# Optimization experiments

Measured on AMD Instinct MI355X. Metric: run time of the kernel, lower is better.

The kernel has to match this reference:

```python
import jax, jax.numpy as jnp
import numpy as np

B, S, D, H = 2, 2048, 1024, 16
HD = D // H
EPS = 1e-5


def setup_inputs() -> dict:
    key = jax.random.key(0)
    ks = jax.random.split(key, 8)
    std = 1.0 / np.sqrt(D)
    x = jax.random.normal(ks[0], (B, S, D), dtype=jnp.float32)
    # causal mask: True = attend (masked_fill where mask==0)
    attention_mask = jnp.tril(jnp.ones((S, S), dtype=bool))[None, None].repeat(B, axis=0)
    return {
        "x": x,
        "attention_mask": attention_mask,
        "ln_gamma": jnp.ones((D,), jnp.float32),
        "ln_beta": jnp.zeros((D,), jnp.float32),
        "w_qkv": jax.random.uniform(ks[1], (D, 3 * D), jnp.float32, -std, std),
        "b_qkv": jnp.zeros((3 * D,), jnp.float32),
        "w_gate": jax.random.uniform(ks[2], (D, D), jnp.float32, -std, std),
        "b_gate": jnp.zeros((D,), jnp.float32),
        "w_out": jax.random.uniform(ks[3], (D, D), jnp.float32, -std, std),
        "b_out": jnp.zeros((D,), jnp.float32),
        "rel_pos_bias": jnp.zeros((1, H, 1, 1), jnp.float32),
    }


def reference(x, attention_mask, ln_gamma, ln_beta, w_qkv, b_qkv,
              w_gate, b_gate, w_out, b_out, rel_pos_bias):
    # LayerNorm over model dim
    mu = jnp.mean(x, axis=-1, keepdims=True)
    var = jnp.mean(jnp.square(x - mu), axis=-1, keepdims=True)
    xn = (x - mu) * jax.lax.rsqrt(var + EPS) * ln_gamma + ln_beta

    qkv = xn @ w_qkv + b_qkv                      # [B,S,3D]
    qkv = qkv.reshape(B, S, 3, H, HD)
    q = qkv[:, :, 0].transpose(0, 2, 1, 3)        # [B,H,S,HD]
    k = qkv[:, :, 1].transpose(0, 2, 1, 3)
    v = qkv[:, :, 2].transpose(0, 2, 1, 3)

    u = jax.nn.silu(xn @ w_gate + b_gate)         # [B,S,D] SiLU gate

    scale = HD ** -0.5
    scores = jnp.einsum('bhqd,bhkd->bhqk', q * scale, k) + rel_pos_bias
    # masked_fill(mask==0, -inf) then sigmoid == zero out masked entries
    attn = jnp.where(attention_mask, jax.nn.sigmoid(scores), 0.0)
    ctx = jnp.einsum('bhqk,bhkd->bhqd', attn, v)  # [B,H,S,HD]
    ctx = ctx.transpose(0, 2, 1, 3).reshape(B, S, D)

    out = (ctx * u) @ w_out + b_out               # gated output proj
    return x + out                                # dropout=eval identity
```

## Files before the change

kernel.cpp:

```cpp
#include <hip/hip_runtime.h>
#include <hip/hip_bf16.h>
#include <cmath>

#define BB 2
#define SS 2048
#define DD 1024
#define HH 16
#define EPS 1e-5f
#define LOG2E 1.44269504088896f
#define QSCALE (0.125f * LOG2E)

typedef __attribute__((ext_vector_type(8))) short short8;
typedef __attribute__((ext_vector_type(4))) float f32x4;

__device__ inline unsigned short f2bf(float f) {
  union { float f; unsigned int u; } v; v.f = f;
  unsigned int u = v.u;
  unsigned int r = (u + 0x7FFFu + ((u >> 16) & 1u)) >> 16;
  return (unsigned short)r;
}
__device__ inline float bf2f(unsigned short h) {
  union { unsigned int u; float f; } v; v.u = ((unsigned int)h) << 16;
  return v.f;
}
__device__ inline unsigned short f2bf_fast(float f) {
  union { float f; unsigned int u; } v; v.f = f;
  return (unsigned short)((v.u + 0x8000u) >> 16);
}

__global__ __launch_bounds__(256) void ln_kernel(
    const float* __restrict__ x, const float* __restrict__ gamma,
    const float* __restrict__ beta, unsigned short* __restrict__ xn) {
  int row = blockIdx.x;
  int t = threadIdx.x;
  const float* xr = x + (size_t)row * DD;
  float4 v = *(const float4*)(xr + t * 4);
  float s = v.x + v.y + v.z + v.w;
  float sq = v.x * v.x + v.y * v.y + v.z * v.z + v.w * v.w;
  for (int off = 32; off > 0; off >>= 1) {
    s += __shfl_down(s, off, 64);
    sq += __shfl_down(sq, off, 64);
  }
  __shared__ float ls[4], lq[4];
  int wave = t >> 6, lane = t & 63;
  if (lane == 0) { ls[wave] = s; lq[wave] = sq; }
  __syncthreads();
  float tot = ls[0] + ls[1] + ls[2] + ls[3];
  float totq = lq[0] + lq[1] + lq[2] + lq[3];
  float mu = tot * (1.0f / DD);
  float var = totq * (1.0f / DD) - mu * mu;
  float rstd = rsqrtf(var + EPS);
  float4 g = *(const float4*)(gamma + t * 4);
  float4 bt = *(const float4*)(beta + t * 4);
  ushort4 o;
  o.x = f2bf((v.x - mu) * rstd * g.x + bt.x);
  o.y = f2bf((v.y - mu) * rstd * g.y + bt.y);
  o.z = f2bf((v.z - mu) * rstd * g.z + bt.z);
  o.w = f2bf((v.w - mu) * rstd * g.w + bt.w);
  *(ushort4*)(xn + (size_t)row * DD + t * 4) = o;
}

__global__ __launch_bounds__(256) void wtrans_all(
    const float* __restrict__ wq, const float* __restrict__ wg,
    const float* __restrict__ wo, unsigned short* __restrict__ wcatT,
    unsigned short* __restrict__ woutT) {
  __shared__ unsigned short tile[32][33];
  int bx = blockIdx.x;
  const float* W;
  unsigned short* Wt;
  int N, colbase;
  if (bx < 96)       { W = wq; Wt = wcatT; N = 3072; colbase = bx * 32; }
  else if (bx < 128) { W = wg; Wt = wcatT + (size_t)3072 * 1024; N = 1024; colbase = (bx - 96) * 32; }
  else               { W = wo; Wt = woutT; N = 1024; colbase = (bx - 128) * 32; }
  int by = blockIdx.y * 32;
  int tx = threadIdx.x & 31, ty = threadIdx.x >> 5;
#pragma unroll
  for (int i = 0; i < 32; i += 8)
    tile[ty + i][tx] = f2bf(W[(size_t)(by + ty + i) * N + colbase + tx]);
  __syncthreads();
#pragma unroll
  for (int i = 0; i < 32; i += 8)
    Wt[(size_t)(colbase + ty + i) * 1024 + by + tx] = tile[tx][ty + i];
}

__global__ __launch_bounds__(256) void gemm_qkvg(
    const unsigned short* __restrict__ A, const unsigned short* __restrict__ Bt,
    const float* __restrict__ bqkv, const float* __restrict__ bgate,
    unsigned short* __restrict__ qkb, unsigned short* __restrict__ vTb,
    unsigned short* __restrict__ ub) {
  __shared__ unsigned short SH[128 * 64];
  unsigned short* As = SH;
  unsigned short* Bs = SH + 128 * 32;
  const int K = 1024;
  int tid = threadIdx.x;
  int wave = tid >> 6, lane = tid & 63;
  int quad = lane >> 4, m16 = lane & 15;
  int wm = wave >> 1, wn = wave & 1;
  int m0 = blockIdx.y * 128, n0 = blockIdx.x * 128;

  int lrow = tid >> 2;
  int lcol = (tid & 3) * 8;
  const unsigned short* Ar0 = A + (size_t)(m0 + lrow) * K + lcol;
  const unsigned short* Ar1 = A + (size_t)(m0 + lrow + 64) * K + lcol;
  const unsigned short* Br0 = Bt + (size_t)(n0 + lrow) * K + lcol;
  const unsigned short* Br1 = Bt + (size_t)(n0 + lrow + 64) * K + lcol;

  f32x4 acc[4][4];
#pragma unroll
  for (int i = 0; i < 4; ++i)
#pragma unroll
    for (int j = 0; j < 4; ++j) acc[i][j] = (f32x4){0.f, 0.f, 0.f, 0.f};

  uint4 a0 = *(const uint4*)Ar0;
  uint4 a1 = *(const uint4*)Ar1;
  uint4 b0 = *(const uint4*)Br0;
  uint4 b1 = *(const uint4*)Br1;

  for (int k0 = 0; k0 < K; k0 += 32) {
    __syncthreads();
    *(uint4*)&As[lrow * 32 + lcol] = a0;
    *(uint4*)&As[(lrow + 64) * 32 + lcol] = a1;
    *(uint4*)&Bs[lrow * 32 + lcol] = b0;
    *(uint4*)&Bs[(lrow + 64) * 32 + lcol] = b1;
    __syncthreads();
    if (k0 + 32 < K) {
      a0 = *(const uint4*)(Ar0 + k0 + 32);
      a1 = *(const uint4*)(Ar1 + k0 + 32);
      b0 = *(const uint4*)(Br0 + k0 + 32);
      b1 = *(const uint4*)(Br1 + k0 + 32);
    }
    short8 af[4], bfr[4];
#pragma unroll
    for (int mi = 0; mi < 4; ++mi)
      af[mi] = *(const short8*)&As[(wm * 64 + mi * 16 + m16) * 32 + quad * 8];
#pragma unroll
    for (int ni = 0; ni < 4; ++ni)
      bfr[ni] = *(const short8*)&Bs[(wn * 64 + ni * 16 + m16) * 32 + quad * 8];
#pragma unroll
    for (int mi = 0; mi < 4; ++mi)
#pragma unroll
      for (int ni = 0; ni < 4; ++ni)
        acc[mi][ni] = __builtin_amdgcn_mfma_f32_16x16x32_bf16(
            af[mi], bfr[ni], acc[mi][ni], 0, 0, 0);
  }

  int sec = n0 >> 10;
  if (sec == 2) {
    int bat = m0 >> 11;
    int s_base = m0 & 2047;
    int dgbase = n0 - 2048;
#pragma unroll
    for (int p = 0; p < 2; ++p) {
      __syncthreads();
      if (wn == p) {
#pragma unroll
        for (int ni = 0; ni < 4; ++ni) {
          int dl = ni * 16 + m16;
          float bb = bqkv[2048 + dgbase + p * 64 + dl];
#pragma unroll
          for (int mi = 0; mi < 4; ++mi)
#pragma unroll
            for (int r = 0; r < 4; ++r) {
              int sl = wm * 64 + mi * 16 + quad * 4 + r;
              int sls = sl ^ ((dl & 7) << 4);
              SH[dl * 128 + sls] = f2bf(acc[mi][ni][r] + bb);
            }
        }
      }
      __syncthreads();
      int dl = tid >> 2;
      int dg = dgbase + p * 64 + dl;
      unsigned short* dst =
          vTb + ((size_t)(bat * 16 + (dg >> 6)) * 64 + (dg & 63)) * 2048 + s_base;
#pragma unroll
      for (int i = 0; i < 4; ++i) {
        int s0 = (tid & 3) * 8 + i * 32;
        int s0s = s0 ^ ((dl & 7) << 4);
        *(uint4*)(dst + s0) = *(const uint4*)&SH[dl * 128 + s0s];
      }
    }
  } else {
    int nwin = n0 + wn * 64;
    if (sec <= 1) {
      float qs = (sec == 0) ? QSCALE : 1.0f;
#pragma unroll
      for (int ni = 0; ni < 4; ++ni) {
        int col = nwin + ni * 16 + m16;
        float bb = bqkv[col];
#pragma unroll
        for (int mi = 0; mi < 4; ++mi)
#pragma unroll
          for (int r = 0; r < 4; ++r) {
            int row = m0 + wm * 64 + mi * 16 + quad * 4 + r;
            qkb[(size_t)row * 2048 + col] = f2bf((acc[mi][ni][r] + bb) * qs);
          }
      }
    } else {
#pragma unroll
      for (int ni = 0; ni < 4; ++ni) {
        int col = nwin + ni * 16 + m16;
        int g = col - 3072;
        float bb = bgate[g];
#pragma unroll
        for (int mi = 0; mi < 4; ++mi)
#pragma unroll
          for (int r = 0; r < 4; ++r) {
            int row = m0 + wm * 64 + mi * 16 + quad * 4 + r;
            float v = acc[mi][ni][r] + bb;
            v = v * __builtin_amdgcn_rcpf(1.0f + exp2f(-v * LOG2E));
            ub[(size_t)row * 1024 + g] = f2bf(v);
          }
      }
    }
  }
}

__global__ __launch_bounds__(256) void gemm_out(
    const unsigned short* __restrict__ A, const unsigned short* __restrict__ Bt,
    const float* __restrict__ bias, const float* __restrict__ resid,
    float* __restrict__ C) {
  __shared__ unsigned short As[128 * 32];
  __shared__ unsigned short Bs[128 * 32];
  const int K = 1024, N = 1024;
  int tid = threadIdx.x;
  int wave = tid >> 6, lane = tid & 63;
  int quad = lane >> 4, m16 = lane & 15;
  int wm = wave >> 1, wn = wave & 1;
  int m0 = blockIdx.y * 128, n0 = blockIdx.x * 128;
  int lrow = tid >> 2;
  int lcol = (tid & 3) * 8;
  const unsigned short* Ar0 = A + (size_t)(m0 + lrow) * K + lcol;
  const unsigned short* Ar1 = A + (size_t)(m0 + lrow + 64) * K + lcol;
  const unsigned short* Br0 = Bt + (size_t)(n0 + lrow) * K + lcol;
  const unsigned short* Br1 = Bt + (size_t)(n0 + lrow + 64) * K + lcol;

  f32x4 acc[4][4];
#pragma unroll
  for (int i = 0; i < 4; ++i)
#pragma unroll
    for (int j = 0; j < 4; ++j) acc[i][j] = (f32x4){0.f, 0.f, 0.f, 0.f};

  uint4 a0 = *(const uint4*)Ar0;
  uint4 a1 = *(const uint4*)Ar1;
  uint4 b0 = *(const uint4*)Br0;
  uint4 b1 = *(const uint4*)Br1;

  for (int k0 = 0; k0 < K; k0 += 32) {
    __syncthreads();
    *(uint4*)&As[lrow * 32 + lcol] = a0;
    *(uint4*)&As[(lrow + 64) * 32 + lcol] = a1;
    *(uint4*)&Bs[lrow * 32 + lcol] = b0;
    *(uint4*)&Bs[(lrow + 64) * 32 + lcol] = b1;
    __syncthreads();
    if (k0 + 32 < K) {
      a0 = *(const uint4*)(Ar0 + k0 + 32);
      a1 = *(const uint4*)(Ar1 + k0 + 32);
      b0 = *(const uint4*)(Br0 + k0 + 32);
      b1 = *(const uint4*)(Br1 + k0 + 32);
    }
    short8 af[4], bfr[4];
#pragma unroll
    for (int mi = 0; mi < 4; ++mi)
      af[mi] = *(const short8*)&As[(wm * 64 + mi * 16 + m16) * 32 + quad * 8];
#pragma unroll
    for (int ni = 0; ni < 4; ++ni)
      bfr[ni] = *(const short8*)&Bs[(wn * 64 + ni * 16 + m16) * 32 + quad * 8];
#pragma unroll
    for (int mi = 0; mi < 4; ++mi)
#pragma unroll
      for (int ni = 0; ni < 4; ++ni)
        acc[mi][ni] = __builtin_amdgcn_mfma_f32_16x16x32_bf16(
            af[mi], bfr[ni], acc[mi][ni], 0, 0, 0);
  }
#pragma unroll
  for (int ni = 0; ni < 4; ++ni) {
    int col = n0 + wn * 64 + ni * 16 + m16;
    float bb = bias[col];
#pragma unroll
    for (int mi = 0; mi < 4; ++mi)
#pragma unroll
      for (int r = 0; r < 4; ++r) {
        int row = m0 + wm * 64 + mi * 16 + quad * 4 + r;
        C[(size_t)row * N + col] =
            acc[mi][ni][r] + bb + resid[(size_t)row * N + col];
      }
  }
}

__global__ __launch_bounds__(256) void attn_mfma(
    const unsigned short* __restrict__ qk, const unsigned short* __restrict__ vT,
    const float* __restrict__ rpb,
    unsigned short* __restrict__ ctx0, unsigned short* __restrict__ ctx1) {
  __shared__ unsigned short Ks[64 * 72];
  __shared__ unsigned short Vs[64 * 72];
  __shared__ unsigned short Ps[64 * 72];

  int qtA = blockIdx.x;
  int qtB = 31 - qtA;
  int q0A = qtA * 64, q0B = qtB * 64;
  int bh = blockIdx.y;
  int sk = blockIdx.z;
  int b = bh >> 4, h = bh & 15;
  int t = threadIdx.x;
  int wave = t >> 6, lane = t & 63;
  int quad = lane >> 4, m16 = lane & 15;

  const unsigned short* qbase = qk + (size_t)(b * SS) * 2048 + h * 64;
  const unsigned short* kbase = qbase + 1024;
  const unsigned short* vbase = vT + (size_t)bh * 64 * 2048;

  int row = t >> 3, blk8 = (t & 7) * 8;

  short8 qfA[2], qfB[2];
#pragma unroll
  for (int s = 0; s < 2; ++s) {
    qfA[s] = *(const short8*)(qbase + (size_t)(q0A + wave * 16 + m16) * 2048 + s * 32 + quad * 8);
    qfB[s] = *(const short8*)(qbase + (size_t)(q0B + wave * 16 + m16) * 2048 + s * 32 + quad * 8);
  }

  f32x4 zero4 = {0.f, 0.f, 0.f, 0.f};
  f32x4 caccA[4], caccB[4];
#pragma unroll
  for (int nb = 0; nb < 4; ++nb) { caccA[nb] = zero4; caccB[nb] = zero4; }

  float hb2 = rpb[h] * LOG2E;
  float cexp = exp2f(-hb2);
  int ktmax = qtB;
  int psw = quad << 3;
  int psr = ((m16 >> 2) & 3) << 3;

  uint4 kv0, kv1, vv0, vv1;
  {
    int k00 = sk * 64;
    const unsigned short* kp = kbase + (size_t)(k00 + row) * 2048 + blk8;
    const unsigned short* vp = vbase + (size_t)row * 2048 + k00 + blk8;
    kv0 = *(const uint4*)kp;
    kv1 = *(const uint4*)(kp + (size_t)32 * 2048);
    vv0 = *(const uint4*)vp;
    vv1 = *(const uint4*)(vp + (size_t)32 * 2048);
  }

  for (int kt = sk; kt <= ktmax; kt += 2) {
    int k0 = kt * 64;
    __syncthreads();
    *(uint4*)&Ks[row * 72 + blk8] = kv0;
    *(uint4*)&Ks[(row + 32) * 72 + blk8] = kv1;
    *(uint4*)&Vs[row * 72 + blk8] = vv0;
    *(uint4*)&Vs[(row + 32) * 72 + blk8] = vv1;
    __syncthreads();
    if (kt + 2 <= ktmax) {
      int k0n = k0 + 128;
      const unsigned short* kp = kbase + (size_t)(k0n + row) * 2048 + blk8;
      const unsigned short* vp = vbase + (size_t)row * 2048 + k0n + blk8;
      kv0 = *(const uint4*)kp;
      kv1 = *(const uint4*)(kp + (size_t)32 * 2048);
      vv0 = *(const uint4*)vp;
      vv1 = *(const uint4*)(vp + (size_t)32 * 2048);
    }

#pragma unroll
    for (int tile = 0; tile < 2; ++tile) {
      if (tile == 1 && kt > qtA) break;
      const short8* qf = (tile == 0) ? qfB : qfA;
      int q0 = (tile == 0) ? q0B : q0A;
      bool diag = (tile == 0) ? (kt == qtB) : (kt == qtA);
      f32x4* cacc = (tile == 0) ? caccB : caccA;

      f32x4 sacc[4];
#pragma unroll
      for (int nb = 0; nb < 4; ++nb) sacc[nb] = zero4;
#pragma unroll
      for (int s = 0; s < 2; ++s) {
#pragma unroll
        for (int nb = 0; nb < 4; ++nb) {
          short8 bf = *(const short8*)&Ks[(nb * 16 + m16) * 72 + s * 32 + quad * 8];
          sacc[nb] = __builtin_amdgcn_mfma_f32_16x16x32_bf16(qf[s], bf, sacc[nb], 0, 0, 0);
        }
      }
#pragma unroll
      for (int nb = 0; nb < 4; ++nb) {
#pragma unroll
        for (int r = 0; r < 4; ++r) {
          float e = exp2f(-sacc[nb][r]);
          float p = __builtin_amdgcn_rcpf(fmaf(cexp, e, 1.0f));
          if (diag) {
            int key = k0 + nb * 16 + m16;
            int q = q0 + wave * 16 + quad * 4 + r;
            if (key > q) p = 0.f;
          }
          int colS = (nb * 16 + m16) ^ psw;
          Ps[(wave * 16 + quad * 4 + r) * 72 + colS] = f2bf_fast(p);
        }
      }
#pragma unroll
      for (int s = 0; s < 2; ++s) {
        int pcol = (s * 32 + quad * 8) ^ psr;
        short8 a = *(const short8*)&Ps[(wave * 16 + m16) * 72 + pcol];
#pragma unroll
        for (int nb = 0; nb < 4; ++nb) {
          short8 bf = *(const short8*)&Vs[(nb * 16 + m16) * 72 + s * 32 + quad * 8];
          cacc[nb] = __builtin_amdgcn_mfma_f32_16x16x32_bf16(a, bf, cacc[nb], 0, 0, 0);
        }
      }
    }
  }

  unsigned short* cp = (sk == 0) ? ctx0 : ctx1;
  unsigned short* cp_ = cp + (size_t)(b * SS) * 1024 + h * 64;
#pragma unroll
  for (int nb = 0; nb < 4; ++nb) {
    int d = nb * 16 + m16;
#pragma unroll
    for (int r = 0; r < 4; ++r) {
      int qA = q0A + wave * 16 + quad * 4 + r;
      int qB = q0B + wave * 16 + quad * 4 + r;
      cp_[(size_t)qA * 1024 + d] = f2bf(caccA[nb][r]);
      cp_[(size_t)qB * 1024 + d] = f2bf(caccB[nb][r]);
    }
  }
}

__global__ __launch_bounds__(256) void combine_kernel(
    const unsigned short* __restrict__ c0, const unsigned short* __restrict__ c1,
    const unsigned short* __restrict__ u, unsigned short* __restrict__ prod) {
  size_t i = ((size_t)blockIdx.x * 256 + threadIdx.x) * 8;
  uint4 a = *(const uint4*)(c0 + i);
  uint4 b = *(const uint4*)(c1 + i);
  uint4 uu = *(const uint4*)(u + i);
  const unsigned short* ae = (const unsigned short*)&a;
  const unsigned short* be = (const unsigned short*)&b;
  const unsigned short* ue = (const unsigned short*)&uu;
  uint4 o;
  unsigned short* oe = (unsigned short*)&o;
#pragma unroll
  for (int j = 0; j < 8; ++j)
    oe[j] = f2bf((bf2f(ae[j]) + bf2f(be[j])) * bf2f(ue[j]));
  *(uint4*)(prod + i) = o;
}

extern "C" void kernel_launch(void* const* d_in, const int* in_sizes, int n_in,
                              void* d_out, int out_size, void* d_ws, size_t ws_size,
                              hipStream_t stream) {
  const float* x      = (const float*)d_in[0];
  const float* gamma  = (const float*)d_in[2];
  const float* beta   = (const float*)d_in[3];
  const float* w_qkv  = (const float*)d_in[4];
  const float* b_qkv  = (const float*)d_in[5];
  const float* w_gate = (const float*)d_in[6];
  const float* b_gate = (const float*)d_in[7];
  const float* w_out  = (const float*)d_in[8];
  const float* b_out  = (const float*)d_in[9];
  const float* rpb    = (const float*)d_in[10];
  float* out = (float*)d_out;

  unsigned short* xnb   = (unsigned short*)d_ws;
  unsigned short* qkb   = xnb + 4194304;
  unsigned short* vTb   = qkb + 8388608;
  unsigned short* ub    = vTb + 4194304;
  unsigned short* prodb = ub + 4194304;
  unsigned short* ctx0b = prodb + 4194304;
  unsigned short* ctx1b = ctx0b + 4194304;
  unsigned short* wcatT = ctx1b + 4194304;
  unsigned short* woutT = wcatT + 4194304;

  ln_kernel<<<BB * SS, 256, 0, stream>>>(x, gamma, beta, xnb);
  wtrans_all<<<dim3(160, 32), 256, 0, stream>>>(w_qkv, w_gate, w_out, wcatT, woutT);
  gemm_qkvg<<<dim3(4096 / 128, 4096 / 128), 256, 0, stream>>>(
      xnb, wcatT, b_qkv, b_gate, qkb, vTb, ub);
  attn_mfma<<<dim3(16, BB * HH, 2), 256, 0, stream>>>(qkb, vTb, rpb, ctx0b, ctx1b);
  combine_kernel<<<4194304 / (256 * 8), 256, 0, stream>>>(ctx0b, ctx1b, ub, prodb);
  gemm_out<<<dim3(1024 / 128, 4096 / 128), 256, 0, stream>>>(
      prodb, woutT, b_out, x, out);
}
```

Baseline: 249.7 us.

## Merge prep kernels, fuse combine into out-proj GEMM, deepen QKV GEMM K-step

New measurement: 356.7 us. 42.8% more time.

```diff
diff --git a/kernel.cpp b/kernel.cpp
--- a/kernel.cpp
+++ b/kernel.cpp
@@ -28,59 +28,61 @@
   return (unsigned short)((v.u + 0x8000u) >> 16);
 }
 
-__global__ __launch_bounds__(256) void ln_kernel(
+__global__ __launch_bounds__(256) void prep_kernel(
     const float* __restrict__ x, const float* __restrict__ gamma,
-    const float* __restrict__ beta, unsigned short* __restrict__ xn) {
-  int row = blockIdx.x;
-  int t = threadIdx.x;
-  const float* xr = x + (size_t)row * DD;
-  float4 v = *(const float4*)(xr + t * 4);
-  float s = v.x + v.y + v.z + v.w;
-  float sq = v.x * v.x + v.y * v.y + v.z * v.z + v.w * v.w;
-  for (int off = 32; off > 0; off >>= 1) {
-    s += __shfl_down(s, off, 64);
-    sq += __shfl_down(sq, off, 64);
-  }
-  __shared__ float ls[4], lq[4];
-  int wave = t >> 6, lane = t & 63;
-  if (lane == 0) { ls[wave] = s; lq[wave] = sq; }
-  __syncthreads();
-  float tot = ls[0] + ls[1] + ls[2] + ls[3];
-  float totq = lq[0] + lq[1] + lq[2] + lq[3];
-  float mu = tot * (1.0f / DD);
-  float var = totq * (1.0f / DD) - mu * mu;
-  float rstd = rsqrtf(var + EPS);
-  float4 g = *(const float4*)(gamma + t * 4);
-  float4 bt = *(const float4*)(beta + t * 4);
-  ushort4 o;
-  o.x = f2bf((v.x - mu) * rstd * g.x + bt.x);
-  o.y = f2bf((v.y - mu) * rstd * g.y + bt.y);
-  o.z = f2bf((v.z - mu) * rstd * g.z + bt.z);
-  o.w = f2bf((v.w - mu) * rstd * g.w + bt.w);
-  *(ushort4*)(xn + (size_t)row * DD + t * 4) = o;
-}
-
-__global__ __launch_bounds__(256) void wtrans_all(
+    const float* __restrict__ beta, unsigned short* __restrict__ xn,
     const float* __restrict__ wq, const float* __restrict__ wg,
     const float* __restrict__ wo, unsigned short* __restrict__ wcatT,
     unsigned short* __restrict__ woutT) {
+  __shared__ float ls[4], lq[4];
   __shared__ unsigned short tile[32][33];
-  int bx = blockIdx.x;
-  const float* W;
-  unsigned short* Wt;
-  int N, colbase;
-  if (bx < 96)       { W = wq; Wt = wcatT; N = 3072; colbase = bx * 32; }
-  else if (bx < 128) { W = wg; Wt = wcatT + (size_t)3072 * 1024; N = 1024; colbase = (bx - 96) * 32; }
-  else               { W = wo; Wt = woutT; N = 1024; colbase = (bx - 128) * 32; }
-  int by = blockIdx.y * 32;
-  int tx = threadIdx.x & 31, ty = threadIdx.x >> 5;
-#pragma unroll
-  for (int i = 0; i < 32; i += 8)
-    tile[ty + i][tx] = f2bf(W[(size_t)(by + ty + i) * N + colbase + tx]);
-  __syncthreads();
-#pragma unroll
-  for (int i = 0; i < 32; i += 8)
-    Wt[(size_t)(colbase + ty + i) * 1024 + by + tx] = tile[tx][ty + i];
+  int bid = blockIdx.x;
+  int t = threadIdx.x;
+  if (bid < 4096) {
+    int row = bid;
+    const float* xr = x + (size_t)row * DD;
+    float4 v = *(const float4*)(xr + t * 4);
+    float s = v.x + v.y + v.z + v.w;
+    float sq = v.x * v.x + v.y * v.y + v.z * v.z + v.w * v.w;
+    for (int off = 32; off > 0; off >>= 1) {
+      s += __shfl_down(s, off, 64);
+      sq += __shfl_down(sq, off, 64);
+    }
+    int wave = t >> 6, lane = t & 63;
+    if (lane == 0) { ls[wave] = s; lq[wave] = sq; }
+    __syncthreads();
+    float tot = ls[0] + ls[1] + ls[2] + ls[3];
+    float totq = lq[0] + lq[1] + lq[2] + lq[3];
+    float mu = tot * (1.0f / DD);
+    float var = totq * (1.0f / DD) - mu * mu;
+    float rstd = rsqrtf(var + EPS);
+    float4 g = *(const float4*)(gamma + t * 4);
+    float4 bt = *(const float4*)(beta + t * 4);
+    ushort4 o;
+    o.x = f2bf((v.x - mu) * rstd * g.x + bt.x);
+    o.y = f2bf((v.y - mu) * rstd * g.y + bt.y);
+    o.z = f2bf((v.z - mu) * rstd * g.z + bt.z);
+    o.w = f2bf((v.w - mu) * rstd * g.w + bt.w);
+    *(ushort4*)(xn + (size_t)row * DD + t * 4) = o;
+  } else {
+    int wb = bid - 4096;
+    int bx = wb % 160;
+    int by = (wb / 160) * 32;
+    const float* W;
+    unsigned short* Wt;
+    int N, colbase;
+    if (bx < 96)       { W = wq; Wt = wcatT; N = 3072; colbase = bx * 32; }
+    else if (bx < 128) { W = wg; Wt = wcatT + (size_t)3072 * 1024; N = 1024; colbase = (bx - 96) * 32; }
+    else               { W = wo; Wt = woutT; N = 1024; colbase = (bx - 128) * 32; }
+    int tx = t & 31, ty = t >> 5;
+#pragma unroll
+    for (int i = 0; i < 32; i += 8)
+      tile[ty + i][tx] = f2bf(W[(size_t)(by + ty + i) * N + colbase + tx]);
+    __syncthreads();
+#pragma unroll
+    for (int i = 0; i < 32; i += 8)
+      Wt[(size_t)(colbase + ty + i) * 1024 + by + tx] = tile[tx][ty + i];
+  }
 }
 
 __global__ __launch_bounds__(256) void gemm_qkvg(
@@ -88,9 +90,8 @@
     const float* __restrict__ bqkv, const float* __restrict__ bgate,
     unsigned short* __restrict__ qkb, unsigned short* __restrict__ vTb,
     unsigned short* __restrict__ ub) {
-  __shared__ unsigned short SH[128 * 64];
-  unsigned short* As = SH;
-  unsigned short* Bs = SH + 128 * 32;
+  __shared__ unsigned short As[2 * 128 * 32];
+  __shared__ unsigned short Bs[2 * 128 * 32];
   const int K = 1024;
   int tid = threadIdx.x;
   int wave = tid >> 6, lane = tid & 63;
@@ -98,12 +99,11 @@
   int wm = wave >> 1, wn = wave & 1;
   int m0 = blockIdx.y * 128, n0 = blockIdx.x * 128;
 
-  int lrow = tid >> 2;
-  int lcol = (tid & 3) * 8;
-  const unsigned short* Ar0 = A + (size_t)(m0 + lrow) * K + lcol;
-  const unsigned short* Ar1 = A + (size_t)(m0 + lrow + 64) * K + lcol;
-  const unsigned short* Br0 = Bt + (size_t)(n0 + lrow) * K + lcol;
-  const unsigned short* Br1 = Bt + (size_t)(n0 + lrow + 64) * K + lcol;
+  int srow = tid >> 3;
+  int scol = (tid & 7) * 8;
+  int sh = scol >> 5;
+  int sc = scol & 31;
+  int sdst = sh * 4096 + srow * 32 + sc;
 
   f32x4 acc[4][4];
 #pragma unroll
@@ -111,41 +111,49 @@
 #pragma unroll
     for (int j = 0; j < 4; ++j) acc[i][j] = (f32x4){0.f, 0.f, 0.f, 0.f};
 
-  uint4 a0 = *(const uint4*)Ar0;
-  uint4 a1 = *(const uint4*)Ar1;
-  uint4 b0 = *(const uint4*)Br0;
-  uint4 b1 = *(const uint4*)Br1;
-
-  for (int k0 = 0; k0 < K; k0 += 32) {
-    __syncthreads();
-    *(uint4*)&As[lrow * 32 + lcol] = a0;
-    *(uint4*)&As[(lrow + 64) * 32 + lcol] = a1;
-    *(uint4*)&Bs[lrow * 32 + lcol] = b0;
-    *(uint4*)&Bs[(lrow + 64) * 32 + lcol] = b1;
-    __syncthreads();
-    if (k0 + 32 < K) {
-      a0 = *(const uint4*)(Ar0 + k0 + 32);
-      a1 = *(const uint4*)(Ar1 + k0 + 32);
-      b0 = *(const uint4*)(Br0 + k0 + 32);
-      b1 = *(const uint4*)(Br1 + k0 + 32);
-    }
-    short8 af[4], bfr[4];
-#pragma unroll
-    for (int mi = 0; mi < 4; ++mi)
-      af[mi] = *(const short8*)&As[(wm * 64 + mi * 16 + m16) * 32 + quad * 8];
-#pragma unroll
-    for (int ni = 0; ni < 4; ++ni)
-      bfr[ni] = *(const short8*)&Bs[(wn * 64 + ni * 16 + m16) * 32 + quad * 8];
-#pragma unroll
-    for (int mi = 0; mi < 4; ++mi)
+  uint4 pa[4], pb[4];
+#pragma unroll
+  for (int g = 0; g < 4; ++g) {
+    pa[g] = *(const uint4*)(A + (size_t)(m0 + srow + 32 * g) * K + scol);
+    pb[g] = *(const uint4*)(Bt + (size_t)(n0 + srow + 32 * g) * K + scol);
+  }
+
+  for (int k0 = 0; k0 < K; k0 += 64) {
+    __syncthreads();
+#pragma unroll
+    for (int g = 0; g < 4; ++g) {
+      *(uint4*)&As[sdst + g * 1024] = pa[g];
+      *(uint4*)&Bs[sdst + g * 1024] = pb[g];
+    }
+    __syncthreads();
+    if (k0 + 64 < K) {
+#pragma unroll
+      for (int g = 0; g < 4; ++g) {
+        pa[g] = *(const uint4*)(A + (size_t)(m0 + srow + 32 * g) * K + k0 + 64 + scol);
+        pb[g] = *(const uint4*)(Bt + (size_t)(n0 + srow + 32 * g) * K + k0 + 64 + scol);
+      }
+    }
+#pragma unroll
+    for (int s = 0; s < 2; ++s) {
+      short8 af[4], bfr[4];
+#pragma unroll
+      for (int mi = 0; mi < 4; ++mi)
+        af[mi] = *(const short8*)&As[s * 4096 + (wm * 64 + mi * 16 + m16) * 32 + quad * 8];
 #pragma unroll
       for (int ni = 0; ni < 4; ++ni)
-        acc[mi][ni] = __builtin_amdgcn_mfma_f32_16x16x32_bf16(
-            af[mi], bfr[ni], acc[mi][ni], 0, 0, 0);
+        bfr[ni] = *(const short8*)&Bs[s * 4096 + (wn * 64 + ni * 16 + m16) * 32 + quad * 8];
+#pragma unroll
+      for (int mi = 0; mi < 4; ++mi)
+#pragma unroll
+        for (int ni = 0; ni < 4; ++ni)
+          acc[mi][ni] = __builtin_amdgcn_mfma_f32_16x16x32_bf16(
+              af[mi], bfr[ni], acc[mi][ni], 0, 0, 0);
+    }
   }
 
   int sec = n0 >> 10;
   if (sec == 2) {
+    unsigned short* SH = As;
     int bat = m0 >> 11;
     int s_base = m0 & 2047;
     int dgbase = n0 - 2048;
@@ -212,78 +220,6 @@
           }
       }
     }
-  }
-}
-
-__global__ __launch_bounds__(256) void gemm_out(
-    const unsigned short* __restrict__ A, const unsigned short* __restrict__ Bt,
-    const float* __restrict__ bias, const float* __restrict__ resid,
-    float* __restrict__ C) {
-  __shared__ unsigned short As[128 * 32];
-  __shared__ unsigned short Bs[128 * 32];
-  const int K = 1024, N = 1024;
-  int tid = threadIdx.x;
-  int wave = tid >> 6, lane = tid & 63;
-  int quad = lane >> 4, m16 = lane & 15;
-  int wm = wave >> 1, wn = wave & 1;
-  int m0 = blockIdx.y * 128, n0 = blockIdx.x * 128;
-  int lrow = tid >> 2;
-  int lcol = (tid & 3) * 8;
-  const unsigned short* Ar0 = A + (size_t)(m0 + lrow) * K + lcol;
-  const unsigned short* Ar1 = A + (size_t)(m0 + lrow + 64) * K + lcol;
-  const unsigned short* Br0 = Bt + (size_t)(n0 + lrow) * K + lcol;
-  const unsigned short* Br1 = Bt + (size_t)(n0 + lrow + 64) * K + lcol;
-
-  f32x4 acc[4][4];
-#pragma unroll
-  for (int i = 0; i < 4; ++i)
-#pragma unroll
-    for (int j = 0; j < 4; ++j) acc[i][j] = (f32x4){0.f, 0.f, 0.f, 0.f};
-
-  uint4 a0 = *(const uint4*)Ar0;
-  uint4 a1 = *(const uint4*)Ar1;
-  uint4 b0 = *(const uint4*)Br0;
-  uint4 b1 = *(const uint4*)Br1;
-
-  for (int k0 = 0; k0 < K; k0 += 32) {
-    __syncthreads();
-    *(uint4*)&As[lrow * 32 + lcol] = a0;
-    *(uint4*)&As[(lrow + 64) * 32 + lcol] = a1;
-    *(uint4*)&Bs[lrow * 32 + lcol] = b0;
-    *(uint4*)&Bs[(lrow + 64) * 32 + lcol] = b1;
-    __syncthreads();
-    if (k0 + 32 < K) {
-      a0 = *(const uint4*)(Ar0 + k0 + 32);
-      a1 = *(const uint4*)(Ar1 + k0 + 32);
-      b0 = *(const uint4*)(Br0 + k0 + 32);
-      b1 = *(const uint4*)(Br1 + k0 + 32);
-    }
-    short8 af[4], bfr[4];
-#pragma unroll
-    for (int mi = 0; mi < 4; ++mi)
-      af[mi] = *(const short8*)&As[(wm * 64 + mi * 16 + m16) * 32 + quad * 8];
-#pragma unroll
-    for (int ni = 0; ni < 4; ++ni)
-      bfr[ni] = *(const short8*)&Bs[(wn * 64 + ni * 16 + m16) * 32 + quad * 8];
-#pragma unroll
-    for (int mi = 0; mi < 4; ++mi)
-#pragma unroll
-      for (int ni = 0; ni < 4; ++ni)
-        acc[mi][ni] = __builtin_amdgcn_mfma_f32_16x16x32_bf16(
-            af[mi], bfr[ni], acc[mi][ni], 0, 0, 0);
-  }
-#pragma unroll
-  for (int ni = 0; ni < 4; ++ni) {
-    int col = n0 + wn * 64 + ni * 16 + m16;
-    float bb = bias[col];
-#pragma unroll
-    for (int mi = 0; mi < 4; ++mi)
-#pragma unroll
-      for (int r = 0; r < 4; ++r) {
-        int row = m0 + wm * 64 + mi * 16 + quad * 4 + r;
-        C[(size_t)row * N + col] =
-            acc[mi][ni][r] + bb + resid[(size_t)row * N + col];
-      }
   }
 }
 
@@ -420,22 +356,89 @@
   }
 }
 
-__global__ __launch_bounds__(256) void combine_kernel(
+__global__ __launch_bounds__(256) void gemm_out(
     const unsigned short* __restrict__ c0, const unsigned short* __restrict__ c1,
-    const unsigned short* __restrict__ u, unsigned short* __restrict__ prod) {
-  size_t i = ((size_t)blockIdx.x * 256 + threadIdx.x) * 8;
-  uint4 a = *(const uint4*)(c0 + i);
-  uint4 b = *(const uint4*)(c1 + i);
-  uint4 uu = *(const uint4*)(u + i);
-  const unsigned short* ae = (const unsigned short*)&a;
-  const unsigned short* be = (const unsigned short*)&b;
-  const unsigned short* ue = (const unsigned short*)&uu;
-  uint4 o;
-  unsigned short* oe = (unsigned short*)&o;
-#pragma unroll
-  for (int j = 0; j < 8; ++j)
-    oe[j] = f2bf((bf2f(ae[j]) + bf2f(be[j])) * bf2f(ue[j]));
-  *(uint4*)(prod + i) = o;
+    const unsigned short* __restrict__ u, const unsigned short* __restrict__ Bt,
+    const float* __restrict__ bias, const float* __restrict__ resid,
+    float* __restrict__ C) {
+  __shared__ unsigned short As[64 * 32];
+  __shared__ unsigned short Bs[128 * 32];
+  const int K = 1024, N = 1024;
+  int tid = threadIdx.x;
+  int wave = tid >> 6, lane = tid & 63;
+  int quad = lane >> 4, m16 = lane & 15;
+  int wm = wave >> 1, wn = wave & 1;
+  int m0 = blockIdx.y * 64, n0 = blockIdx.x * 128;
+
+  int arow = tid >> 2, acol = (tid & 3) * 8;
+  const unsigned short* c0p = c0 + (size_t)(m0 + arow) * K + acol;
+  const unsigned short* c1p = c1 + (size_t)(m0 + arow) * K + acol;
+  const unsigned short* up  = u  + (size_t)(m0 + arow) * K + acol;
+  const unsigned short* Br0 = Bt + (size_t)(n0 + arow) * K + acol;
+  const unsigned short* Br1 = Bt + (size_t)(n0 + arow + 64) * K + acol;
+
+  f32x4 acc[2][4];
+#pragma unroll
+  for (int i = 0; i < 2; ++i)
+#pragma unroll
+    for (int j = 0; j < 4; ++j) acc[i][j] = (f32x4){0.f, 0.f, 0.f, 0.f};
+
+  uint4 p0 = *(const uint4*)c0p;
+  uint4 p1 = *(const uint4*)c1p;
+  uint4 pu = *(const uint4*)up;
+  uint4 pb0 = *(const uint4*)Br0;
+  uint4 pb1 = *(const uint4*)Br1;
+
+  for (int k0 = 0; k0 < K; k0 += 32) {
+    uint4 af4;
+    {
+      const unsigned short* e0 = (const unsigned short*)&p0;
+      const unsigned short* e1 = (const unsigned short*)&p1;
+      const unsigned short* eu = (const unsigned short*)&pu;
+      unsigned short* ea = (unsigned short*)&af4;
+#pragma unroll
+      for (int j = 0; j < 8; ++j)
+        ea[j] = f2bf((bf2f(e0[j]) + bf2f(e1[j])) * bf2f(eu[j]));
+    }
+    __syncthreads();
+    *(uint4*)&As[arow * 32 + acol] = af4;
+    *(uint4*)&Bs[arow * 32 + acol] = pb0;
+    *(uint4*)&Bs[(arow + 64) * 32 + acol] = pb1;
+    __syncthreads();
+    if (k0 + 32 < K) {
+      p0 = *(const uint4*)(c0p + k0 + 32);
+      p1 = *(const uint4*)(c1p + k0 + 32);
+      pu = *(const uint4*)(up + k0 + 32);
+      pb0 = *(const uint4*)(Br0 + k0 + 32);
+      pb1 = *(const uint4*)(Br1 + k0 + 32);
+    }
+    short8 af[2], bfr[4];
+#pragma unroll
+    for (int mi = 0; mi < 2; ++mi)
+      af[mi] = *(const short8*)&As[(wm * 32 + mi * 16 + m16) * 32 + quad * 8];
+#pragma unroll
+    for (int ni = 0; ni < 4; ++ni)
+      bfr[ni] = *(const short8*)&Bs[(wn * 64 + ni * 16 + m16) * 32 + quad * 8];
+#pragma unroll
+    for (int mi = 0; mi < 2; ++mi)
+#pragma unroll
+      for (int ni = 0; ni < 4; ++ni)
+        acc[mi][ni] = __builtin_amdgcn_mfma_f32_16x16x32_bf16(
+            af[mi], bfr[ni], acc[mi][ni], 0, 0, 0);
+  }
+#pragma unroll
+  for (int ni = 0; ni < 4; ++ni) {
+    int col = n0 + wn * 64 + ni * 16 + m16;
+    float bb = bias[col];
+#pragma unroll
+    for (int mi = 0; mi < 2; ++mi)
+#pragma unroll
+      for (int r = 0; r < 4; ++r) {
+        int rowi = m0 + wm * 32 + mi * 16 + quad * 4 + r;
+        C[(size_t)rowi * N + col] =
+            acc[mi][ni][r] + bb + resid[(size_t)rowi * N + col];
+      }
+  }
 }
 
 extern "C" void kernel_launch(void* const* d_in, const int* in_sizes, int n_in,
@@ -457,18 +460,16 @@
   unsigned short* qkb   = xnb + 4194304;
   unsigned short* vTb   = qkb + 8388608;
   unsigned short* ub    = vTb + 4194304;
-  unsigned short* prodb = ub + 4194304;
-  unsigned short* ctx0b = prodb + 4194304;
+  unsigned short* ctx0b = ub + 4194304;
   unsigned short* ctx1b = ctx0b + 4194304;
   unsigned short* wcatT = ctx1b + 4194304;
   unsigned short* woutT = wcatT + 4194304;
 
-  ln_kernel<<<BB * SS, 256, 0, stream>>>(x, gamma, beta, xnb);
-  wtrans_all<<<dim3(160, 32), 256, 0, stream>>>(w_qkv, w_gate, w_out, wcatT, woutT);
+  prep_kernel<<<4096 + 5120, 256, 0, stream>>>(
+      x, gamma, beta, xnb, w_qkv, w_gate, w_out, wcatT, woutT);
   gemm_qkvg<<<dim3(4096 / 128, 4096 / 128), 256, 0, stream>>>(
       xnb, wcatT, b_qkv, b_gate, qkb, vTb, ub);
   attn_mfma<<<dim3(16, BB * HH, 2), 256, 0, stream>>>(qkb, vTb, rpb, ctx0b, ctx1b);
-  combine_kernel<<<4194304 / (256 * 8), 256, 0, stream>>>(ctx0b, ctx1b, ub, prodb);
-  gemm_out<<<dim3(1024 / 128, 4096 / 128), 256, 0, stream>>>(
-      prodb, woutT, b_out, x, out);
-}
+  gemm_out<<<dim3(1024 / 128, 4096 / 64), 256, 0, stream>>>(
+      ctx0b, ctx1b, ub, woutT, b_out, x, out);
+}
```
